# Kernel tuning notes

Measured on AMD Instinct MI355X. Metric: run time of the kernel, lower is better.

## Reference

```python
import jax, jax.numpy as jnp
import numpy as np

EPS = 1e-15
LRELU_ALPHA = 0.2  # = init alpha


def setup_inputs() -> dict:
    key = jax.random.key(0)
    k1, k2, k3, k4 = jax.random.split(key, 4)
    N, E, F_in, F_out = 100000, 3200000, 256, 64
    inputs = jax.random.normal(k1, (N, F_in), dtype=jnp.float32)
    edge_index = jax.random.randint(k2, (2, E), 0, N, dtype=jnp.int64)
    # xavier_normal with gain 1.414
    W = jax.random.normal(k3, (F_in, F_out), dtype=jnp.float32) * (1.414 * np.sqrt(2.0 / (F_in + F_out)))
    a = jax.random.normal(k4, (1, 2 * F_out), dtype=jnp.float32) * (1.414 * np.sqrt(2.0 / (1 + 2 * F_out)))
    return {"inputs": inputs, "edge_index": edge_index, "W": W, "a": a}


def reference(inputs, edge_index, W, a):
    N = inputs.shape[0]
    F_out = W.shape[1]
    src = edge_index[0]  # row i (destination of aggregation)
    dst = edge_index[1]  # col j (neighbor being aggregated)

    h = inputs @ W  # [N, F_out]
    # values = a @ concat(h[src], h[dst]).T  ==  (h @ a1)[src] + (h @ a2)[dst]
    a1 = a[0, :F_out]
    a2 = a[0, F_out:]
    s1 = h @ a1  # [N]
    s2 = h @ a2  # [N]
    values = s1[src] + s2[dst]  # [E]
    ev_a = jax.nn.leaky_relu(values, LRELU_ALPHA)
    edge_value = jnp.exp(ev_a - jnp.max(ev_a))  # global max, as in torch code

    # e_rowsum = A @ ones  -> per-row sum of edge values
    e_rowsum = jax.ops.segment_sum(edge_value, src, num_segments=N)  # [N]
    # h_prime = A @ h (dropout p=0 -> identity)
    h_prime = jax.ops.segment_sum(edge_value[:, None] * h[dst], src, num_segments=N)  # [N, F_out]
    h_prime = h_prime / (e_rowsum[:, None] + EPS)
    return jax.nn.elu(h_prime)  # concat=True
```

## Files before the change

### kernel.cpp

```cpp
#include <hip/hip_runtime.h>
#include <hip/hip_bf16.h>
#include <math.h>

#define F_IN 256
#define F_OUT 64
#define LRELU_ALPHA 0.2f
#define EPS 1e-15f
#define CHUNK 8192
#define BSH 7
#define BNODES 128
#define NBMAX 1024
#define LCAP 4800

typedef __bf16 bf16x8 __attribute__((ext_vector_type(8)));
typedef float  f32x4  __attribute__((ext_vector_type(4)));

__device__ __forceinline__ unsigned int fkey(float x) {
    unsigned int u = __float_as_uint(x);
    return (u & 0x80000000u) ? ~u : (u | 0x80000000u);
}
__device__ __forceinline__ float funkey(unsigned int k) {
    return (k & 0x80000000u) ? __uint_as_float(k ^ 0x80000000u)
                             : __uint_as_float(~k);
}
__device__ __forceinline__ unsigned short f2bf(float x) {
    __hip_bfloat16 b = __float2bfloat16(x);
    return *reinterpret_cast<unsigned short*>(&b);
}
__device__ __forceinline__ float bf2f(unsigned int u) {
    return __uint_as_float(u << 16);
}

__global__ __launch_bounds__(256) void wprep(
    const float* __restrict__ W, unsigned short* __restrict__ Wt)
{
    const int i = blockIdx.x * 256 + threadIdx.x;
    const int n = i & 63;
    const int k = i >> 6;
    Wt[n * 256 + k] = f2bf(W[k * 64 + n]);
}

#define KAP 72
__global__ __launch_bounds__(256) void gemm_part(
    const float* __restrict__ X, const unsigned short* __restrict__ Wt,
    const float* __restrict__ a,
    unsigned short* __restrict__ h_bf, float* __restrict__ s1,
    float* __restrict__ s2, unsigned int* __restrict__ gsmax, int N,
    const int* __restrict__ src, const int* __restrict__ dst,
    int* __restrict__ coarse_cnt, unsigned int* __restrict__ coarse,
    int E, int NB, int GB)
{
    __shared__ __align__(16) char smem[18464];

    if (blockIdx.x < GB) {
        unsigned short* As = (unsigned short*)smem;
        float* red1 = (float*)(smem + 18432);
        float* red2 = red1 + 4;

        const int tid  = threadIdx.x;
        const int lane = tid & 63;
        const int l15  = lane & 15;
        const int quad = lane >> 4;
        const int w    = tid >> 6;
        const int n0   = blockIdx.x * 128;

        const unsigned short* wbase = Wt + l15 * 256 + quad * 8;

        f32x4 acc[2][4] = {};

        for (int c = 0; c < 4; ++c) {
            __syncthreads();
#pragma unroll
            for (int i = 0; i < 8; ++i) {
                int q   = tid + i * 256;
                int row = q >> 4;
                int k4  = q & 15;
                int gr  = n0 + row;
                float4 v = make_float4(0.f, 0.f, 0.f, 0.f);
                if (gr < N)
                    v = *(const float4*)&X[(size_t)gr * F_IN + c * 64 + k4 * 4];
                unsigned int p0 = f2bf(v.x) | ((unsigned int)f2bf(v.y) << 16);
                unsigned int p1 = f2bf(v.z) | ((unsigned int)f2bf(v.w) << 16);
                *(uint2*)&As[row * KAP + k4 * 4] = make_uint2(p0, p1);
            }
            __syncthreads();

#pragma unroll
            for (int ks = 0; ks < 64; ks += 32) {
                bf16x8 afrag[2], bfrag[4];
#pragma unroll
                for (int rt = 0; rt < 2; ++rt) {
                    uint4 ua = *(const uint4*)&As[(w * 32 + rt * 16 + l15) * KAP + ks + quad * 8];
                    afrag[rt] = __builtin_bit_cast(bf16x8, ua);
                }
#pragma unroll
                for (int ct = 0; ct < 4; ++ct) {
                    uint4 ub = *(const uint4*)&wbase[ct * 4096 + c * 64 + ks];
                    bfrag[ct] = __builtin_bit_cast(bf16x8, ub);
                }
#pragma unroll
                for (int rt = 0; rt < 2; ++rt)
#pragma unroll
                    for (int ct = 0; ct < 4; ++ct)
                        acc[rt][ct] = __builtin_amdgcn_mfma_f32_16x16x32_bf16(
                            afrag[rt], bfrag[ct], acc[rt][ct], 0, 0, 0);
            }
        }

        float a1v[4], a2v[4];
#pragma unroll
        for (int ct = 0; ct < 4; ++ct) {
            a1v[ct] = a[ct * 16 + l15];
            a2v[ct] = a[F_OUT + ct * 16 + l15];
        }
        float m1 = -INFINITY, m2 = -INFINITY;
#pragma unroll
        for (int rt = 0; rt < 2; ++rt) {
#pragma unroll
            for (int reg = 0; reg < 4; ++reg) {
                int n = n0 + w * 32 + rt * 16 + quad * 4 + reg;
                float p1 = 0.f, p2 = 0.f;
#pragma unroll
                for (int ct = 0; ct < 4; ++ct) {
                    float v = acc[rt][ct][reg];
                    p1 = fmaf(v, a1v[ct], p1);
                    p2 = fmaf(v, a2v[ct], p2);
                }
#pragma unroll
                for (int ofs = 1; ofs < 16; ofs <<= 1) {
                    p1 += __shfl_xor(p1, ofs, 64);
                    p2 += __shfl_xor(p2, ofs, 64);
                }
                if (n < N) {
#pragma unroll
                    for (int ct = 0; ct < 4; ++ct)
                        h_bf[(size_t)n * F_OUT + ct * 16 + l15] = f2bf(acc[rt][ct][reg]);
                    if (l15 == 0) { s1[n] = p1; s2[n] = p2; }
                    m1 = fmaxf(m1, p1);
                    m2 = fmaxf(m2, p2);
                }
            }
        }
#pragma unroll
        for (int ofs = 32; ofs > 0; ofs >>= 1) {
            m1 = fmaxf(m1, __shfl_xor(m1, ofs, 64));
            m2 = fmaxf(m2, __shfl_xor(m2, ofs, 64));
        }
        if (lane == 0) { red1[w] = m1; red2[w] = m2; }
        __syncthreads();
        if (tid == 0) {
            float b1 = fmaxf(fmaxf(red1[0], red1[1]), fmaxf(red1[2], red1[3]));
            float b2 = fmaxf(fmaxf(red2[0], red2[1]), fmaxf(red2[2], red2[3]));
            atomicMax(&gsmax[0], fkey(b1));
            atomicMax(&gsmax[1], fkey(b2));
        }
    } else {
        int* hist = (int*)smem;
        int* cur  = hist + NBMAX;
        const int pb = blockIdx.x - GB;
        const int e0 = pb * CHUNK;
        const int e1 = (e0 + CHUNK < E) ? e0 + CHUNK : E;

        for (int i = threadIdx.x; i < NB; i += 256) hist[i] = 0;
        __syncthreads();
        for (int e = e0 + threadIdx.x; e < e1; e += 256)
            atomicAdd(&hist[src[e] >> BSH], 1);
        __syncthreads();
        for (int i = threadIdx.x; i < NB; i += 256) {
            int c = hist[i];
            cur[i] = c ? atomicAdd(&coarse_cnt[i], c) : 0;
        }
        __syncthreads();
        for (int e = e0 + threadIdx.x; e < e1; e += 256) {
            int s = src[e], d = dst[e];
            int b = s >> BSH;
            int pos = atomicAdd(&cur[b], 1);
            if (pos < LCAP)
                coarse[(size_t)b * LCAP + pos] =
                    ((unsigned int)d << BSH) | (unsigned int)(s & (BNODES - 1));
        }
    }
}

__global__ __launch_bounds__(512) void bin_gather(
    const unsigned int* __restrict__ coarse, const int* __restrict__ coarse_cnt,
    const float* __restrict__ s1, const float* __restrict__ s2,
    const unsigned int* __restrict__ gsmax,
    const unsigned short* __restrict__ hb, float* __restrict__ out, int N)
{
    __shared__ unsigned int leds[LCAP];
    __shared__ int   hcnt[BNODES];
    __shared__ int   hinc[BNODES];
    __shared__ int   curs[BNODES];
    __shared__ float s1s[BNODES];

    const int b  = blockIdx.x;
    const int t  = threadIdx.x;
    const int n0 = b << BSH;
    int cnt = coarse_cnt[b];
    if (cnt > LCAP) cnt = LCAP;
    const unsigned int* cb = coarse + (size_t)b * LCAP;

    if (t < BNODES) {
        hcnt[t] = 0;
        s1s[t] = (n0 + t < N) ? s1[n0 + t] : 0.f;
    }
    __syncthreads();

    for (int e = t; e < cnt; e += 512)
        atomicAdd(&hcnt[cb[e] & (BNODES - 1)], 1);
    __syncthreads();

    if (t < BNODES) hinc[t] = hcnt[t];
    __syncthreads();
    for (int d = 1; d < BNODES; d <<= 1) {
        int x = (t < BNODES && t >= d) ? hinc[t - d] : 0;
        __syncthreads();
        if (t < BNODES) hinc[t] += x;
        __syncthreads();
    }
    if (t < BNODES) curs[t] = hinc[t] - hcnt[t];
    __syncthreads();

    const float M = funkey(gsmax[0]) + funkey(gsmax[1]);
    for (int e = t; e < cnt; e += 512) {
        unsigned int p = cb[e];
        int sl = p & (BNODES - 1);
        int d  = p >> BSH;
        float v = s1s[sl] + s2[d];
        v = fmaxf(v, LRELU_ALPHA * v);
        float w = __expf(v - M);
        unsigned int wb = f2bf(w);
        int pos = atomicAdd(&curs[sl], 1);
        leds[pos] = ((unsigned int)d << 15) | wb;
    }
    __syncthreads();

    const int lane = t & 63;
    const int wv   = t >> 6;
    const int g    = lane >> 4;
    const int fi   = lane & 15;

    for (int i = 0; i < 16; ++i) {
        const int nl = wv * 16 + i;
        const int n  = n0 + nl;
        const bool valid = (n < N);
        const int re = valid ? hinc[nl] : 0;
        const int rs = valid ? re - hcnt[nl] : 0;

        float a0 = 0.f, a1 = 0.f, a2 = 0.f, a3 = 0.f, ws = 0.f;
        for (int bb = rs; bb < re; bb += 64) {
            const int nb = (re - bb < 64) ? re - bb : 64;
            unsigned int pv = (lane < nb) ? leds[bb + lane] : 0u;
            ws += bf2f(pv & 0x7fffu);
            for (int k = 0; k < nb; k += 4) {
                unsigned int pe = __shfl(pv, k + g, 64);
                float w = bf2f(pe & 0x7fffu);
                uint2 hv = *(const uint2*)&hb[(size_t)(pe >> 15) * F_OUT + fi * 4];
                a0 = fmaf(w, bf2f(hv.x & 0xffffu), a0);
                a1 = fmaf(w, bf2f(hv.x >> 16),     a1);
                a2 = fmaf(w, bf2f(hv.y & 0xffffu), a2);
                a3 = fmaf(w, bf2f(hv.y >> 16),     a3);
            }
        }
        a0 += __shfl_xor(a0, 16, 64); a0 += __shfl_xor(a0, 32, 64);
        a1 += __shfl_xor(a1, 16, 64); a1 += __shfl_xor(a1, 32, 64);
        a2 += __shfl_xor(a2, 16, 64); a2 += __shfl_xor(a2, 32, 64);
        a3 += __shfl_xor(a3, 16, 64); a3 += __shfl_xor(a3, 32, 64);
#pragma unroll
        for (int ofs = 32; ofs > 0; ofs >>= 1)
            ws += __shfl_xor(ws, ofs, 64);

        if (valid && g == 0) {
            float inv = 1.f / (ws + EPS);
            float x0 = a0 * inv, x1 = a1 * inv, x2 = a2 * inv, x3 = a3 * inv;
            x0 = (x0 > 0.f) ? x0 : expm1f(x0);
            x1 = (x1 > 0.f) ? x1 : expm1f(x1);
            x2 = (x2 > 0.f) ? x2 : expm1f(x2);
            x3 = (x3 > 0.f) ? x3 : expm1f(x3);
            *(float4*)&out[(size_t)n * F_OUT + fi * 4] = make_float4(x0, x1, x2, x3);
        }
    }
}

extern "C" void kernel_launch(void* const* d_in, const int* in_sizes, int n_in,
                              void* d_out, int out_size, void* d_ws, size_t ws_size,
                              hipStream_t stream) {
    const float* X   = (const float*)d_in[0];
    const int*   ei  = (const int*)d_in[1];
    const float* W   = (const float*)d_in[2];
    const float* a   = (const float*)d_in[3];
    float*       out = (float*)d_out;

    const int N = in_sizes[0] / F_IN;
    const int E = in_sizes[1] / 2;
    const int* src = ei;
    const int* dst = ei + E;

    const int NB = (N + BNODES - 1) >> BSH;
    const int GB = (N + 127) / 128;
    const int PB = (E + CHUNK - 1) / CHUNK;

    unsigned short* h_bf = (unsigned short*)d_ws;
    float* s1         = (float*)(h_bf + (size_t)N * F_OUT);
    float* s2         = s1 + N;
    int*   coarse_cnt = (int*)(s2 + N);
    unsigned int* gsmax = (unsigned int*)(coarse_cnt + NB);
    unsigned short* Wt = (unsigned short*)(gsmax + 2);
    unsigned int* coarse = (unsigned int*)(Wt + 64 * 256);

    hipMemsetAsync(coarse_cnt, 0, ((size_t)NB + 2) * sizeof(int), stream);

    wprep     <<<64, 256, 0, stream>>>(W, Wt);
    gemm_part <<<GB + PB, 256, 0, stream>>>(X, Wt, a, h_bf, s1, s2, gsmax, N,
                                            src, dst, coarse_cnt, coarse,
                                            E, NB, GB);
    bin_gather<<<NB, 512, 0, stream>>>(coarse, coarse_cnt, s1, s2, gsmax,
                                       h_bf, out, N);
}
```

Baseline: 365.0 us.

## Vectorize edge binning loads, pad global bin counters, halve partition chunk size

The partition blocks now read src/dst as int4 vectors and unroll the per-edge atomic binning four-wide, with a scalar tail loop. Each global per-bin counter is padded to its own 64-byte slot (CPAD=16) to reduce atomic contention and false sharing. CHUNK is halved, which doubles the number of partition blocks for more parallelism but also doubles the number of global atomics per bin. The int4 loads assume src+e0 and dst+e0 are 16-byte aligned, which holds only when E is a multiple of 4.

```diff
diff --git a/kernel.cpp b/kernel.cpp
--- a/kernel.cpp
+++ b/kernel.cpp
@@ -6,11 +6,12 @@
 #define F_OUT 64
 #define LRELU_ALPHA 0.2f
 #define EPS 1e-15f
-#define CHUNK 8192
+#define CHUNK 4096
 #define BSH 7
 #define BNODES 128
 #define NBMAX 1024
 #define LCAP 4800
+#define CPAD 16
 
 typedef __bf16 bf16x8 __attribute__((ext_vector_type(8)));
 typedef float  f32x4  __attribute__((ext_vector_type(4)));
@@ -160,25 +161,52 @@
         const int pb = blockIdx.x - GB;
         const int e0 = pb * CHUNK;
         const int e1 = (e0 + CHUNK < E) ? e0 + CHUNK : E;
+        const int nv = (e1 - e0) >> 2;
+        const int4* s4p = (const int4*)(src + e0);
+        const int4* d4p = (const int4*)(dst + e0);
 
         for (int i = threadIdx.x; i < NB; i += 256) hist[i] = 0;
         __syncthreads();
-        for (int e = e0 + threadIdx.x; e < e1; e += 256)
+
+        for (int i = threadIdx.x; i < nv; i += 256) {
+            int4 s4 = s4p[i];
+            atomicAdd(&hist[s4.x >> BSH], 1);
+            atomicAdd(&hist[s4.y >> BSH], 1);
+            atomicAdd(&hist[s4.z >> BSH], 1);
+            atomicAdd(&hist[s4.w >> BSH], 1);
+        }
+        for (int e = e0 + (nv << 2) + threadIdx.x; e < e1; e += 256)
             atomicAdd(&hist[src[e] >> BSH], 1);
         __syncthreads();
+
         for (int i = threadIdx.x; i < NB; i += 256) {
             int c = hist[i];
-            cur[i] = c ? atomicAdd(&coarse_cnt[i], c) : 0;
-        }
-        __syncthreads();
-        for (int e = e0 + threadIdx.x; e < e1; e += 256) {
+            cur[i] = c ? atomicAdd(&coarse_cnt[(size_t)i * CPAD], c) : 0;
+        }
+        __syncthreads();
+
+        for (int i = threadIdx.x; i < nv; i += 256) {
+            int4 s4 = s4p[i];
+            int4 d4 = d4p[i];
+#define PUT(S, D)                                                          \
+            {                                                              \
+                int b_   = (S) >> BSH;                                     \
+                int pos_ = atomicAdd(&cur[b_], 1);                         \
+                if (pos_ < LCAP)                                           \
+                    coarse[(size_t)b_ * LCAP + pos_] =                     \
+                        ((unsigned int)(D) << BSH) |                       \
+                        (unsigned int)((S) & (BNODES - 1));                \
+            }
+            PUT(s4.x, d4.x)
+            PUT(s4.y, d4.y)
+            PUT(s4.z, d4.z)
+            PUT(s4.w, d4.w)
+        }
+        for (int e = e0 + (nv << 2) + threadIdx.x; e < e1; e += 256) {
             int s = src[e], d = dst[e];
-            int b = s >> BSH;
-            int pos = atomicAdd(&cur[b], 1);
-            if (pos < LCAP)
-                coarse[(size_t)b * LCAP + pos] =
-                    ((unsigned int)d << BSH) | (unsigned int)(s & (BNODES - 1));
-        }
+            PUT(s, d)
+        }
+#undef PUT
     }
 }
 
@@ -197,7 +225,7 @@
     const int b  = blockIdx.x;
     const int t  = threadIdx.x;
     const int n0 = b << BSH;
-    int cnt = coarse_cnt[b];
+    int cnt = coarse_cnt[(size_t)b * CPAD];
     if (cnt > LCAP) cnt = LCAP;
     const unsigned int* cb = coarse + (size_t)b * LCAP;
 
@@ -305,11 +333,11 @@
     float* s1         = (float*)(h_bf + (size_t)N * F_OUT);
     float* s2         = s1 + N;
     int*   coarse_cnt = (int*)(s2 + N);
-    unsigned int* gsmax = (unsigned int*)(coarse_cnt + NB);
+    unsigned int* gsmax = (unsigned int*)(coarse_cnt + (size_t)NB * CPAD);
     unsigned short* Wt = (unsigned short*)(gsmax + 2);
     unsigned int* coarse = (unsigned int*)(Wt + 64 * 256);
 
-    hipMemsetAsync(coarse_cnt, 0, ((size_t)NB + 2) * sizeof(int), stream);
+    hipMemsetAsync(coarse_cnt, 0, ((size_t)NB * CPAD + 2) * sizeof(int), stream);
 
     wprep     <<<64, 256, 0, stream>>>(W, Wt);
     gemm_part <<<GB + PB, 256, 0, stream>>>(X, Wt, a, h_bf, s1, s2, gsmax, N,
```

Result: faster. 332.2 us (-9.0%).
